# Kernel optimization log

Measured on AMD Instinct MI355X. Metric: run time of the kernel, lower is better.

The kernel has to match this reference:

```python
import jax, jax.numpy as jnp
import numpy as np

B, IN_F, NQ, L = 4096, 1024, 4, 2   # batch, in_features, qubits/circuit, entangler layers
C = IN_F // NQ                      # n_circuits = 256


def _rx(theta):
    # RX(theta) = [[cos(t/2), -i sin(t/2)], [-i sin(t/2), cos(t/2)]]
    c = jnp.cos(theta / 2).astype(jnp.complex64)
    s = jnp.sin(theta / 2).astype(jnp.complex64)
    return jnp.stack([jnp.stack([c, -1j * s]), jnp.stack([-1j * s, c])])


def _apply_1q(U, state, q):
    # contract 2x2 gate along qubit axis q of state with shape (2,)*NQ
    return jnp.moveaxis(jnp.tensordot(U, state, axes=([1], [q])), 0, q)


def _cnot(state, ctrl, tgt):
    s0 = jnp.take(state, 0, axis=ctrl)
    s1 = jnp.take(state, 1, axis=ctrl)
    t = tgt - 1 if tgt > ctrl else tgt
    s1 = jnp.flip(s1, axis=t)          # X on target in the ctrl=1 block
    return jnp.stack([s0, s1], axis=ctrl)


def _sim_one(xv, w):
    # xv: (NQ,) input angles; w: (L, NQ) variational angles
    # Angle embedding: RX(x_q) on |0> per qubit -> product state [cos, -i sin]
    cos = jnp.cos(xv / 2).astype(jnp.complex64)
    sin = (-1j) * jnp.sin(xv / 2).astype(jnp.complex64)
    state = jnp.stack([cos[0], sin[0]])
    for q in range(1, NQ):
        state = jnp.tensordot(state, jnp.stack([cos[q], sin[q]]), axes=0)
    # BasicEntanglerLayers: per layer, RX on each wire then ring of CNOTs
    for l in range(L):
        for q in range(NQ):
            state = _apply_1q(_rx(w[l, q]), state, q)
        for q in range(NQ):
            state = _cnot(state, q, (q + 1) % NQ)
    # Measurement: <Z_q> for every wire
    probs = jnp.real(state * jnp.conj(state))
    zsign = jnp.array([1.0, -1.0], jnp.float32)
    zs = [probs.sum(axis=tuple(a for a in range(NQ) if a != q)) @ zsign
          for q in range(NQ)]
    return jnp.stack(zs)


def setup_inputs() -> dict:
    key = jax.random.key(0)
    kx, kw = jax.random.split(key)
    x = jax.random.normal(kx, (B, IN_F), jnp.float32)
    weights = jax.random.uniform(kw, (C, L, NQ), jnp.float32, 0.0, 2.0 * np.pi)
    return {"x": x, "weights": weights}


def reference(x, weights):
    xr = x.reshape(B, C, NQ)
    sim = jax.vmap(jax.vmap(_sim_one, in_axes=(0, 0)), in_axes=(0, None))
    out = sim(xr, weights)                 # (B, C, NQ)
    return out.reshape(B, C * NQ).astype(jnp.float32)
```

## Files before the change

kernel.cpp:

```cpp
#include <hip/hip_runtime.h>
#include <math.h>


#define BQ 4096
#define CQ 256

__global__ __launch_bounds__(256) void qsim_kernel(
    const float* __restrict__ x,
    const float* __restrict__ w,
    float* __restrict__ out)
{
    const int tid = blockIdx.x * blockDim.x + threadIdx.x;
    const int c = tid & (CQ - 1);

    const float4 xv = reinterpret_cast<const float4*>(x)[tid];
    const float4 w0 = reinterpret_cast<const float4*>(w)[c * 2 + 0];
    const float4 w1 = reinterpret_cast<const float4*>(w)[c * 2 + 1];

    float cq[4], sq[4];
    __sincosf((xv.x + w0.x) * 0.5f, &sq[0], &cq[0]);
    __sincosf((xv.y + w0.y) * 0.5f, &sq[1], &cq[1]);
    __sincosf((xv.z + w0.z) * 0.5f, &sq[2], &cq[2]);
    __sincosf((xv.w + w0.w) * 0.5f, &sq[3], &cq[3]);

    float c1[4], s1[4];
    __sincosf(w1.x * 0.5f, &s1[0], &c1[0]);
    __sincosf(w1.y * 0.5f, &s1[1], &c1[1]);
    __sincosf(w1.z * 0.5f, &s1[2], &c1[2]);
    __sincosf(w1.w * 0.5f, &s1[3], &c1[3]);

    float ar[16], ai[16];
#pragma unroll
    for (int n = 0; n < 16; ++n) {
        const float m = ((n & 8) ? sq[0] : cq[0])
                      * ((n & 4) ? sq[1] : cq[1])
                      * ((n & 2) ? sq[2] : cq[2])
                      * ((n & 1) ? sq[3] : cq[3]);
        const int k = ((n & 1) + ((n >> 1) & 1) + ((n >> 2) & 1) + ((n >> 3) & 1)) & 3;
        ar[n] = (k == 0) ? m : ((k == 2) ? -m : 0.0f);
        ai[n] = (k == 1) ? -m : ((k == 3) ? m : 0.0f);
    }

#pragma unroll
    for (int q = 0; q < 4; ++q) {
        const int cm = 8 >> q;
        const int tm = 8 >> ((q + 1) & 3);
#pragma unroll
        for (int n = 0; n < 16; ++n) {
            if ((n & cm) && !(n & tm)) {
                const int n1 = n | tm;
                float t;
                t = ar[n]; ar[n] = ar[n1]; ar[n1] = t;
                t = ai[n]; ai[n] = ai[n1]; ai[n1] = t;
            }
        }
    }

#pragma unroll
    for (int q = 0; q < 4; ++q) {
        const int m = 8 >> q;
        const float cg = c1[q], sg = s1[q];
#pragma unroll
        for (int n = 0; n < 16; ++n) {
            if (!(n & m)) {
                const int n1 = n | m;
                const float a_r = ar[n], a_i = ai[n];
                const float b_r = ar[n1], b_i = ai[n1];
                ar[n]  = cg * a_r + sg * b_i;
                ai[n]  = cg * a_i - sg * b_r;
                ar[n1] = cg * b_r + sg * a_i;
                ai[n1] = cg * b_i - sg * a_r;
            }
        }
    }

#pragma unroll
    for (int q = 0; q < 4; ++q) {
        const int cm = 8 >> q;
        const int tm = 8 >> ((q + 1) & 3);
#pragma unroll
        for (int n = 0; n < 16; ++n) {
            if ((n & cm) && !(n & tm)) {
                const int n1 = n | tm;
                float t;
                t = ar[n]; ar[n] = ar[n1]; ar[n1] = t;
                t = ai[n]; ai[n] = ai[n1]; ai[n1] = t;
            }
        }
    }

    float p[16];
#pragma unroll
    for (int n = 0; n < 16; ++n) p[n] = ar[n] * ar[n] + ai[n] * ai[n];

    float z0 = 0.f, z1 = 0.f, z2 = 0.f, z3 = 0.f;
#pragma unroll
    for (int n = 0; n < 16; ++n) {
        z0 += (n & 8) ? -p[n] : p[n];
        z1 += (n & 4) ? -p[n] : p[n];
        z2 += (n & 2) ? -p[n] : p[n];
        z3 += (n & 1) ? -p[n] : p[n];
    }

    reinterpret_cast<float4*>(out)[tid] = make_float4(z0, z1, z2, z3);
}

extern "C" void kernel_launch(void* const* d_in, const int* in_sizes, int n_in,
                              void* d_out, int out_size, void* d_ws, size_t ws_size,
                              hipStream_t stream) {
    const float* x = (const float*)d_in[0];
    const float* w = (const float*)d_in[1];
    float* out = (float*)d_out;

    const int total = BQ * CQ;
    qsim_kernel<<<total / 256, 256, 0, stream>>>(x, w, out);
}
```

Measured before the change: 80.97 us.

## Fold CNOT permutations into amplitude init and use butterfly Z-expectation reduction

```diff
diff --git a/kernel.cpp b/kernel.cpp
--- a/kernel.cpp
+++ b/kernel.cpp
@@ -17,74 +17,56 @@
     const float4 w0 = reinterpret_cast<const float4*>(w)[c * 2 + 0];
     const float4 w1 = reinterpret_cast<const float4*>(w)[c * 2 + 1];
 
-    float cq[4], sq[4];
-    __sincosf((xv.x + w0.x) * 0.5f, &sq[0], &cq[0]);
-    __sincosf((xv.y + w0.y) * 0.5f, &sq[1], &cq[1]);
-    __sincosf((xv.z + w0.z) * 0.5f, &sq[2], &cq[2]);
-    __sincosf((xv.w + w0.w) * 0.5f, &sq[3], &cq[3]);
+    const float t0 = (xv.x + w0.x) * 0.5f;
+    const float t1 = (xv.y + w0.y) * 0.5f;
+    const float t2 = (xv.z + w0.z) * 0.5f;
+    const float t3 = (xv.w + w0.w) * 0.5f;
+    const float cA = __cosf(t0), sA = __sinf(t0);
+    const float cB = __cosf(t1), sB = __sinf(t1);
+    const float cC = __cosf(t2), sC = __sinf(t2);
+    const float cD = __cosf(t3), sD = __sinf(t3);
 
-    float c1[4], s1[4];
-    __sincosf(w1.x * 0.5f, &s1[0], &c1[0]);
-    __sincosf(w1.y * 0.5f, &s1[1], &c1[1]);
-    __sincosf(w1.z * 0.5f, &s1[2], &c1[2]);
-    __sincosf(w1.w * 0.5f, &s1[3], &c1[3]);
+    float gc[4], gs[4];
+    gc[0] = __cosf(w1.x * 0.5f); gs[0] = __sinf(w1.x * 0.5f);
+    gc[1] = __cosf(w1.y * 0.5f); gs[1] = __sinf(w1.y * 0.5f);
+    gc[2] = __cosf(w1.z * 0.5f); gs[2] = __sinf(w1.z * 0.5f);
+    gc[3] = __cosf(w1.w * 0.5f); gs[3] = __sinf(w1.w * 0.5f);
+
+    float a01[4], a23[4];
+    a01[0] = cA * cB; a01[1] = cA * sB; a01[2] = sA * cB; a01[3] = sA * sB;
+    a23[0] = cC * cD; a23[1] = cC * sD; a23[2] = sC * cD; a23[3] = sC * sD;
+
+    float m[16];
+#pragma unroll
+    for (int n = 0; n < 16; ++n) m[n] = a01[n >> 2] * a23[n & 3];
+
+    constexpr int sp[16]   = {0,13,3,14,6,11,5,8,12,1,15,2,10,7,9,4};
+    constexpr int phi1[16] = {0,1, 2,1, 2,1, 2,3, 2, 3,0, 3,2, 1,2,3};
 
     float ar[16], ai[16];
 #pragma unroll
     for (int n = 0; n < 16; ++n) {
-        const float m = ((n & 8) ? sq[0] : cq[0])
-                      * ((n & 4) ? sq[1] : cq[1])
-                      * ((n & 2) ? sq[2] : cq[2])
-                      * ((n & 1) ? sq[3] : cq[3]);
-        const int k = ((n & 1) + ((n >> 1) & 1) + ((n >> 2) & 1) + ((n >> 3) & 1)) & 3;
-        ar[n] = (k == 0) ? m : ((k == 2) ? -m : 0.0f);
-        ai[n] = (k == 1) ? -m : ((k == 3) ? m : 0.0f);
+        const float r = m[sp[n]];
+        ar[n] = (phi1[n] == 0) ? r : ((phi1[n] == 2) ? -r : 0.0f);
+        ai[n] = (phi1[n] == 1) ? r : ((phi1[n] == 3) ? -r : 0.0f);
     }
 
+    constexpr int gq[4]  = {3, 0, 1, 2};
+    constexpr int gm[4]  = {1, 8, 4, 2};
 #pragma unroll
-    for (int q = 0; q < 4; ++q) {
-        const int cm = 8 >> q;
-        const int tm = 8 >> ((q + 1) & 3);
+    for (int g = 0; g < 4; ++g) {
+        const float cg = gc[gq[g]], sg = gs[gq[g]];
+        const int mk = gm[g];
 #pragma unroll
         for (int n = 0; n < 16; ++n) {
-            if ((n & cm) && !(n & tm)) {
-                const int n1 = n | tm;
-                float t;
-                t = ar[n]; ar[n] = ar[n1]; ar[n1] = t;
-                t = ai[n]; ai[n] = ai[n1]; ai[n1] = t;
-            }
-        }
-    }
-
-#pragma unroll
-    for (int q = 0; q < 4; ++q) {
-        const int m = 8 >> q;
-        const float cg = c1[q], sg = s1[q];
-#pragma unroll
-        for (int n = 0; n < 16; ++n) {
-            if (!(n & m)) {
-                const int n1 = n | m;
-                const float a_r = ar[n], a_i = ai[n];
-                const float b_r = ar[n1], b_i = ai[n1];
-                ar[n]  = cg * a_r + sg * b_i;
-                ai[n]  = cg * a_i - sg * b_r;
-                ar[n1] = cg * b_r + sg * a_i;
-                ai[n1] = cg * b_i - sg * a_r;
-            }
-        }
-    }
-
-#pragma unroll
-    for (int q = 0; q < 4; ++q) {
-        const int cm = 8 >> q;
-        const int tm = 8 >> ((q + 1) & 3);
-#pragma unroll
-        for (int n = 0; n < 16; ++n) {
-            if ((n & cm) && !(n & tm)) {
-                const int n1 = n | tm;
-                float t;
-                t = ar[n]; ar[n] = ar[n1]; ar[n1] = t;
-                t = ai[n]; ai[n] = ai[n1]; ai[n1] = t;
+            if (!(n & mk)) {
+                const int n1 = n | mk;
+                const float r0 = ar[n],  i0 = ai[n];
+                const float r1 = ar[n1], i1 = ai[n1];
+                ar[n]  = cg * r0 + sg * i1;
+                ai[n]  = cg * i0 - sg * r1;
+                ar[n1] = cg * r1 + sg * i0;
+                ai[n1] = cg * i1 - sg * r0;
             }
         }
     }
@@ -93,14 +75,27 @@
 #pragma unroll
     for (int n = 0; n < 16; ++n) p[n] = ar[n] * ar[n] + ai[n] * ai[n];
 
-    float z0 = 0.f, z1 = 0.f, z2 = 0.f, z3 = 0.f;
+    float sAv[8], dAv[8];
 #pragma unroll
-    for (int n = 0; n < 16; ++n) {
-        z0 += (n & 8) ? -p[n] : p[n];
-        z1 += (n & 4) ? -p[n] : p[n];
-        z2 += (n & 2) ? -p[n] : p[n];
-        z3 += (n & 1) ? -p[n] : p[n];
+    for (int k = 0; k < 8; ++k) {
+        sAv[k] = p[2 * k] + p[2 * k + 1];
+        dAv[k] = p[2 * k] - p[2 * k + 1];
     }
+    float dd[4], ss[4], sd[4];
+#pragma unroll
+    for (int j = 0; j < 4; ++j) {
+        dd[j] = dAv[2 * j] - dAv[2 * j + 1];
+        ss[j] = sAv[2 * j] + sAv[2 * j + 1];
+        sd[j] = sAv[2 * j] - sAv[2 * j + 1];
+    }
+    const float g0 = dd[0] - dd[1], g1 = dd[2] - dd[3];
+    const float u0 = ss[0] - ss[1], u1 = ss[2] - ss[3];
+    const float v0 = sd[0] - sd[1], v1 = sd[2] - sd[3];
+
+    const float z0 = g0 + g1;
+    const float z3 = g0 - g1;
+    const float z1 = u0 - u1;
+    const float z2 = v0 - v1;
 
     reinterpret_cast<float4*>(out)[tid] = make_float4(z0, z1, z2, z3);
 }
```

Result: faster. 77.01 us (-4.9%).
